# Performance work log

Measured on AMD Instinct MI355X. Metric: run time of the kernel, lower is better.

The kernel has to match this reference:

```python
import jax, jax.numpy as jnp
import numpy as np
from jax import lax

NPOINT = 1024
RADIUS = 0.2
NSAMPLE = 32
BN_EPS = 1e-5


def farthest_point_sample(xyz, npoint):
    # xyz: (B, N, 3). Deterministic start at index 0 (torch uses randint).
    B, N, _ = xyz.shape

    def step(carry, _):
        distance, farthest = carry
        centroid = jnp.take_along_axis(xyz, farthest[:, None, None], axis=1)  # (B,1,3)
        d = jnp.sum((xyz - centroid) ** 2, axis=-1)  # (B,N)
        distance = jnp.minimum(distance, d)
        return (distance, jnp.argmax(distance, axis=-1).astype(jnp.int32)), farthest

    init = (jnp.full((B, N), 1e10, xyz.dtype), jnp.zeros((B,), jnp.int32))
    _, idxs = lax.scan(step, init, None, length=npoint)  # (npoint, B)
    return jnp.transpose(idxs)  # (B, npoint)


def square_distance(src, dst):
    # src: (B,S,3), dst: (B,N,3) -> (B,S,N) squared distances
    d = -2.0 * jnp.einsum('bsc,bnc->bsn', src, dst)
    d = d + jnp.sum(src ** 2, axis=-1)[:, :, None]
    d = d + jnp.sum(dst ** 2, axis=-1)[:, None, :]
    return d


def query_ball_point(radius, nsample, xyz, new_xyz):
    B, N, _ = xyz.shape
    S = new_xyz.shape[1]
    sqrdists = square_distance(new_xyz, xyz)  # (B,S,N)
    idx = jnp.broadcast_to(jnp.arange(N, dtype=jnp.int32), (B, S, N))
    idx = jnp.where(sqrdists > radius ** 2, N, idx)
    idx = jnp.sort(idx, axis=-1)[:, :, :nsample]  # (B,S,K)
    first = idx[:, :, :1]
    return jnp.where(idx == N, first, idx)


# batched gather: points (B,N,C), idx (B,...) -> (B,...,C)
_gather = jax.vmap(lambda p, i: p[i])


def bn_relu(x, gamma, beta):
    # training-mode BatchNorm2d over (B, C, S, K): stats over axes (0,2,3)
    m = jnp.mean(x, axis=(0, 2, 3), keepdims=True)
    v = jnp.var(x, axis=(0, 2, 3), keepdims=True)
    y = (x - m) * lax.rsqrt(v + BN_EPS)
    return jax.nn.relu(y * gamma[None, :, None, None] + beta[None, :, None, None])


def reference(xyz, points, W0, b0, g0, be0, W1, b1, g1, be1, W2, b2, g2, be2):
    # xyz: (B,3,N), points: (B,C,N)
    xyz_t = jnp.transpose(xyz, (0, 2, 1))      # (B,N,3)
    pts_t = jnp.transpose(points, (0, 2, 1))   # (B,N,C)

    fps_idx = farthest_point_sample(xyz_t, NPOINT)          # (B,S)
    new_xyz = _gather(xyz_t, fps_idx)                        # (B,S,3)
    group_idx = query_ball_point(RADIUS, NSAMPLE, xyz_t, new_xyz)  # (B,S,K)

    grouped_xyz = _gather(xyz_t, group_idx) - new_xyz[:, :, None, :]  # (B,S,K,3)
    grouped_pts = _gather(pts_t, group_idx)                           # (B,S,K,C)
    feat = jnp.concatenate([grouped_xyz, grouped_pts], axis=-1)      # (B,S,K,C+3)

    x = jnp.transpose(feat, (0, 3, 1, 2))  # (B, C+3, S, K)
    for W, b, g, be in ((W0, b0, g0, be0), (W1, b1, g1, be1), (W2, b2, g2, be2)):
        x = bn_relu(jnp.einsum('bcsk,oc->bosk', x, W) + b[None, :, None, None], g, be)
    new_points = jnp.max(x, axis=-1)  # (B, C_out, S)

    return jnp.transpose(new_xyz, (0, 2, 1)), new_points


def setup_inputs() -> dict:
    key = jax.random.key(0)
    ks = jax.random.split(key, 8)
    B, C_in, N = 16, 6, 4096
    inp = {
        'xyz': jax.random.uniform(ks[0], (B, 3, N), dtype=jnp.float32),
        'points': jax.random.normal(ks[1], (B, C_in, N), dtype=jnp.float32),
        'W0': 0.1 * jax.random.normal(ks[2], (32, C_in + 3), dtype=jnp.float32),
        'b0': 0.1 * jax.random.normal(ks[3], (32,), dtype=jnp.float32),
        'g0': jnp.ones((32,), jnp.float32),
        'be0': jnp.zeros((32,), jnp.float32),
        'W1': 0.1 * jax.random.normal(ks[4], (32, 32), dtype=jnp.float32),
        'b1': 0.1 * jax.random.normal(ks[5], (32,), dtype=jnp.float32),
        'g1': jnp.ones((32,), jnp.float32),
        'be1': jnp.zeros((32,), jnp.float32),
        'W2': 0.1 * jax.random.normal(ks[6], (64, 32), dtype=jnp.float32),
        'b2': 0.1 * jax.random.normal(ks[7], (64,), dtype=jnp.float32),
        'g2': jnp.ones((64,), jnp.float32),
        'be2': jnp.zeros((64,), jnp.float32),
    }
    return inp
```

## Files before the change

kernel.cpp:

```cpp
#include <hip/hip_runtime.h>

#define BATCH   16
#define NPTS    4096
#define NPOINT  1024
#define NSAMPLE 32
#define NSITES  (BATCH*NPOINT*NSAMPLE)


__device__ __forceinline__ float wave_max_bcast(float x) {
    int v = __float_as_int(x);
    int t;
    t = __builtin_amdgcn_update_dpp(v, v, 0x111, 0xf, 0xf, false);
    v = __float_as_int(fmaxf(__int_as_float(v), __int_as_float(t)));
    t = __builtin_amdgcn_update_dpp(v, v, 0x112, 0xf, 0xf, false);
    v = __float_as_int(fmaxf(__int_as_float(v), __int_as_float(t)));
    t = __builtin_amdgcn_update_dpp(v, v, 0x114, 0xf, 0xf, false);
    v = __float_as_int(fmaxf(__int_as_float(v), __int_as_float(t)));
    t = __builtin_amdgcn_update_dpp(v, v, 0x118, 0xf, 0xf, false);
    v = __float_as_int(fmaxf(__int_as_float(v), __int_as_float(t)));
    t = __builtin_amdgcn_update_dpp(v, v, 0x142, 0xa, 0xf, false);
    v = __float_as_int(fmaxf(__int_as_float(v), __int_as_float(t)));
    t = __builtin_amdgcn_update_dpp(v, v, 0x143, 0xc, 0xf, false);
    v = __float_as_int(fmaxf(__int_as_float(v), __int_as_float(t)));
    return __int_as_float(__builtin_amdgcn_readlane(v, 63));
}

__global__ __launch_bounds__(512, 1) void fps_kernel(
    const float* __restrict__ xyz,
    float* __restrict__ nxyz,
    float* __restrict__ out0)
{
    __shared__ float sx[NPTS], sy[NPTS], sz[NPTS];
    __shared__ int   s_sel[NPOINT];
    __shared__ unsigned long long redK[2][8];

    const int b = blockIdx.x;
    const int t = threadIdx.x;
    const int wave = t >> 6, lane = t & 63;
    const float* xb = xyz + (size_t)b * 3 * NPTS;

    for (int i = t; i < NPTS; i += 512) {
        sx[i] = xb[i]; sy[i] = xb[NPTS+i]; sz[i] = xb[2*NPTS+i];
    }
    __syncthreads();

    const int base = t * 8;
    float px[8], py[8], pz[8], dist[8];
    #pragma unroll
    for (int j = 0; j < 8; ++j) {
        px[j] = sx[base+j]; py[j] = sy[base+j]; pz[j] = sz[base+j];
        dist[j] = 1e10f;
    }

    int far = 0;
    float cx = sx[0], cy = sy[0], cz = sz[0];
    for (int it = 0; it < NPOINT; ++it) {
        if (t == 0) s_sel[it] = far;
        #pragma unroll
        for (int j = 0; j < 8; ++j) {
            const float dx = __fsub_rn(px[j], cx);
            const float dy = __fsub_rn(py[j], cy);
            const float dz = __fsub_rn(pz[j], cz);
            const float d  = __fadd_rn(__fadd_rn(__fmul_rn(dx,dx), __fmul_rn(dy,dy)),
                                       __fmul_rn(dz,dz));
            dist[j] = fminf(dist[j], d);
        }
        float tv0, tv1, tv2, tv3; int ti0, ti1, ti2, ti3;
        { bool c = dist[1] > dist[0]; tv0 = c ? dist[1] : dist[0]; ti0 = c ? 1 : 0; }
        { bool c = dist[3] > dist[2]; tv1 = c ? dist[3] : dist[2]; ti1 = c ? 3 : 2; }
        { bool c = dist[5] > dist[4]; tv2 = c ? dist[5] : dist[4]; ti2 = c ? 5 : 4; }
        { bool c = dist[7] > dist[6]; tv3 = c ? dist[7] : dist[6]; ti3 = c ? 7 : 6; }
        float nv0, nv1; int ni0, ni1;
        { bool c = tv1 > tv0; nv0 = c ? tv1 : tv0; ni0 = c ? ti1 : ti0; }
        { bool c = tv3 > tv2; nv1 = c ? tv3 : tv2; ni1 = c ? ti3 : ti2; }
        float bm; int bj;
        { bool c = nv1 > nv0; bm = c ? nv1 : nv0; bj = c ? ni1 : ni0; }
        const float M = wave_max_bcast(bm);
        const unsigned long long mask = __ballot(bm == M);
        const int wl = __ffsll(mask) - 1;
        const int par = it & 1;
        if (lane == wl) {
            const unsigned idxg = (unsigned)(base + bj);
            redK[par][wave] = ((unsigned long long)__float_as_uint(M) << 32)
                              | (unsigned)(~idxg);
        }
        __syncthreads();
        const unsigned long long k0 = redK[par][0], k1 = redK[par][1];
        const unsigned long long k2 = redK[par][2], k3 = redK[par][3];
        const unsigned long long k4 = redK[par][4], k5 = redK[par][5];
        const unsigned long long k6 = redK[par][6], k7 = redK[par][7];
        const unsigned long long a0 = (k1 > k0) ? k1 : k0;
        const unsigned long long a1 = (k3 > k2) ? k3 : k2;
        const unsigned long long a2 = (k5 > k4) ? k5 : k4;
        const unsigned long long a3 = (k7 > k6) ? k7 : k6;
        const unsigned long long b0_ = (a1 > a0) ? a1 : a0;
        const unsigned long long b1_ = (a3 > a2) ? a3 : a2;
        const unsigned long long km  = (b1_ > b0_) ? b1_ : b0_;
        far = (int)((~(unsigned)km) & (NPTS-1));
        cx = sx[far]; cy = sy[far]; cz = sz[far];
    }
    __syncthreads();
    for (int s = t; s < NPOINT; s += 512) {
        const int id = s_sel[s];
        const float x = sx[id], y = sy[id], z = sz[id];
        nxyz[((size_t)b*NPOINT + s)*3 + 0] = x;
        nxyz[((size_t)b*NPOINT + s)*3 + 1] = y;
        nxyz[((size_t)b*NPOINT + s)*3 + 2] = z;
        out0[(size_t)b*3*NPOINT + 0*NPOINT + s] = x;
        out0[(size_t)b*3*NPOINT + 1*NPOINT + s] = y;
        out0[(size_t)b*3*NPOINT + 2*NPOINT + s] = z;
    }
}

__global__ __launch_bounds__(256) void ball_kernel(
    const float* __restrict__ xyz, const float* __restrict__ nxyz,
    int* __restrict__ gidx)
{
    __shared__ float sx[NPTS], sy[NPTS], sz[NPTS];
    const int b  = blockIdx.x >> 4;
    const int sg = blockIdx.x & 15;
    const int t = threadIdx.x;
    const int wave = t >> 6, lane = t & 63;
    const float* xb = xyz + (size_t)b * 3 * NPTS;
    for (int i = t; i < NPTS; i += 256) {
        sx[i] = xb[i]; sy[i] = xb[NPTS+i]; sz[i] = xb[2*NPTS+i];
    }
    __syncthreads();
    const unsigned long long lt = (1ull << lane) - 1ull;

    for (int q = wave; q < 64; q += 4) {
        const int s = sg*64 + q;
        const size_t bs = (size_t)b*NPOINT + s;
        const float cx = nxyz[bs*3+0], cy = nxyz[bs*3+1], cz = nxyz[bs*3+2];
        const float ss = __fadd_rn(__fadd_rn(__fmul_rn(cx,cx), __fmul_rn(cy,cy)),
                                   __fmul_rn(cz,cz));
        int* out = gidx + bs*NSAMPLE;
        int cnt = 0;
        int firstIdx = NPTS;
        for (int ch = 0; ch < NPTS/64 && cnt < NSAMPLE; ++ch) {
            const int pi = ch*64 + lane;
            const float qx = sx[pi], qy = sy[pi], qz = sz[pi];
            const float dot = fmaf(cz, qz, fmaf(cy, qy, __fmul_rn(cx, qx)));
            const float sn  = __fadd_rn(__fadd_rn(__fmul_rn(qx,qx), __fmul_rn(qy,qy)),
                                        __fmul_rn(qz,qz));
            const float d   = __fadd_rn(__fadd_rn(__fmul_rn(-2.0f,dot), ss), sn);
            const bool pred = !(d > 0.04f);
            const unsigned long long m = __ballot(pred);
            if (pred) {
                const int pos = cnt + __popcll(m & lt);
                if (pos == 0) firstIdx = pi;
                if (pos < NSAMPLE) out[pos] = pi;
            }
            cnt += (int)__popcll(m);
        }
        if (cnt < NSAMPLE) {
            #pragma unroll
            for (int off = 32; off >= 1; off >>= 1) {
                const int oi = __shfl_xor(firstIdx, off);
                firstIdx = (oi < firstIdx) ? oi : firstIdx;
            }
            for (int p = cnt + lane; p < NSAMPLE; p += 64) out[p] = firstIdx;
        }
    }
}

__device__ __forceinline__ void gather_feat(
    const float* __restrict__ xyz, const float* __restrict__ pts,
    const int* __restrict__ gidx, const float* __restrict__ nxyz,
    int v, float4 f[9])
{
    const int site = v * 4;
    const int bs = site >> 5;
    const int b  = bs >> 10;
    const int4 idx = *reinterpret_cast<const int4*>(gidx + site);
    const float* xb = xyz + (size_t)b*3*NPTS;
    const float* pb = pts + (size_t)b*6*NPTS;
    const float cx = nxyz[(size_t)bs*3+0];
    const float cy = nxyz[(size_t)bs*3+1];
    const float cz = nxyz[(size_t)bs*3+2];
    f[0] = make_float4(xb[idx.x]-cx, xb[idx.y]-cx, xb[idx.z]-cx, xb[idx.w]-cx);
    f[1] = make_float4(xb[NPTS+idx.x]-cy, xb[NPTS+idx.y]-cy, xb[NPTS+idx.z]-cy, xb[NPTS+idx.w]-cy);
    f[2] = make_float4(xb[2*NPTS+idx.x]-cz, xb[2*NPTS+idx.y]-cz, xb[2*NPTS+idx.z]-cz, xb[2*NPTS+idx.w]-cz);
    #pragma unroll
    for (int c = 0; c < 6; ++c)
        f[3+c] = make_float4(pb[c*NPTS+idx.x], pb[c*NPTS+idx.y], pb[c*NPTS+idx.z], pb[c*NPTS+idx.w]);
}

__global__ __launch_bounds__(256) void conv0s_kernel(
    const float* __restrict__ xyz, const float* __restrict__ pts,
    const int* __restrict__ gidx, const float* __restrict__ nxyz,
    const float* __restrict__ W, const float* __restrict__ bias,
    float* __restrict__ xout, float* __restrict__ psum, float* __restrict__ psq)
{
    const int t = threadIdx.x;
    const int v = blockIdx.x*256 + t;
    const int site = v * 4;
    float4 f[9];
    gather_feat(xyz, pts, gidx, nxyz, v, f);
    float acc[32], accq[32];
    #pragma unroll
    for (int o = 0; o < 32; ++o) {
        const float bb = bias[o];
        float4 y = make_float4(bb,bb,bb,bb);
        #pragma unroll
        for (int c = 0; c < 9; ++c) {
            const float w = W[o*9+c];
            y.x = fmaf(w, f[c].x, y.x); y.y = fmaf(w, f[c].y, y.y);
            y.z = fmaf(w, f[c].z, y.z); y.w = fmaf(w, f[c].w, y.w);
        }
        *reinterpret_cast<float4*>(xout + (size_t)o*NSITES + site) = y;
        acc[o]  = (y.x + y.y) + (y.z + y.w);
        accq[o] = (y.x*y.x + y.y*y.y) + (y.z*y.z + y.w*y.w);
    }
    __shared__ float ls[4][32], lq[4][32];
    const int wave = t>>6, lane = t&63;
    #pragma unroll
    for (int o = 0; o < 32; ++o) {
        float s1 = acc[o], q1 = accq[o];
        #pragma unroll
        for (int off = 32; off >= 1; off >>= 1) {
            s1 += __shfl_xor(s1, off);
            q1 += __shfl_xor(q1, off);
        }
        if (lane == 0) { ls[wave][o] = s1; lq[wave][o] = q1; }
    }
    __syncthreads();
    if (t < 32) {
        psum[blockIdx.x*64 + t] = (ls[0][t]+ls[1][t]) + (ls[2][t]+ls[3][t]);
        psq [blockIdx.x*64 + t] = (lq[0][t]+lq[1][t]) + (lq[2][t]+lq[3][t]);
    }
}

__global__ void fold_kernel(
    const float* __restrict__ g, const float* __restrict__ be,
    const float* __restrict__ psum, const float* __restrict__ psq,
    float* __restrict__ aff, int Cout)
{
    const int t = threadIdx.x;
    if (t < Cout) {
        float s = 0.f, q = 0.f;
        for (int i = 0; i < 512; ++i) { s += psum[i*64 + t]; q += psq[i*64 + t]; }
        const float invn = 1.0f / (float)NSITES;
        const float m = s * invn;
        float v2 = fmaxf(q * invn - m*m, 0.f);
        const float a = g[t] * rsqrtf(v2 + 1e-5f);
        aff[t]      = a;
        aff[64 + t] = fmaf(-m, a, be[t]);
    }
}

__global__ __launch_bounds__(256) void conv1s_kernel(
    const float* x, float* xout,
    const float* __restrict__ aff, const float* __restrict__ W,
    const float* __restrict__ bias,
    float* __restrict__ psum, float* __restrict__ psq)
{
    const int t = threadIdx.x;
    const int v = blockIdx.x*256 + t;
    const int site = v * 4;
    float4 in[32];
    #pragma unroll
    for (int c = 0; c < 32; ++c) {
        float4 r = *reinterpret_cast<const float4*>(x + (size_t)c*NSITES + site);
        const float a = aff[c], cc = aff[64 + c];
        in[c].x = fmaxf(fmaf(a, r.x, cc), 0.f);
        in[c].y = fmaxf(fmaf(a, r.y, cc), 0.f);
        in[c].z = fmaxf(fmaf(a, r.z, cc), 0.f);
        in[c].w = fmaxf(fmaf(a, r.w, cc), 0.f);
    }
    float acc[32], accq[32];
    #pragma unroll
    for (int o = 0; o < 32; ++o) {
        const float bb = bias[o];
        float4 y = make_float4(bb,bb,bb,bb);
        #pragma unroll
        for (int c = 0; c < 32; ++c) {
            const float w = W[o*32+c];
            y.x = fmaf(w, in[c].x, y.x); y.y = fmaf(w, in[c].y, y.y);
            y.z = fmaf(w, in[c].z, y.z); y.w = fmaf(w, in[c].w, y.w);
        }
        *reinterpret_cast<float4*>(xout + (size_t)o*NSITES + site) = y;
        acc[o]  = (y.x + y.y) + (y.z + y.w);
        accq[o] = (y.x*y.x + y.y*y.y) + (y.z*y.z + y.w*y.w);
    }
    __shared__ float ls[4][32], lq[4][32];
    const int wave = t>>6, lane = t&63;
    #pragma unroll
    for (int o = 0; o < 32; ++o) {
        float s1 = acc[o], q1 = accq[o];
        #pragma unroll
        for (int off = 32; off >= 1; off >>= 1) {
            s1 += __shfl_xor(s1, off);
            q1 += __shfl_xor(q1, off);
        }
        if (lane == 0) { ls[wave][o] = s1; lq[wave][o] = q1; }
    }
    __syncthreads();
    if (t < 32) {
        psum[blockIdx.x*64 + t] = (ls[0][t]+ls[1][t]) + (ls[2][t]+ls[3][t]);
        psq [blockIdx.x*64 + t] = (lq[0][t]+lq[1][t]) + (lq[2][t]+lq[3][t]);
    }
}

__global__ __launch_bounds__(256) void conv2stats_kernel(
    const float* __restrict__ x, const float* __restrict__ aff,
    const float* __restrict__ W, const float* __restrict__ bias,
    float* __restrict__ psum, float* __restrict__ psq)
{
    const int t = threadIdx.x;
    const int v = blockIdx.x*256 + t;
    const int site = v * 4;
    const int coff = blockIdx.y * 32;
    float4 in[32];
    #pragma unroll
    for (int c = 0; c < 32; ++c) {
        float4 r = *reinterpret_cast<const float4*>(x + (size_t)c*NSITES + site);
        const float a = aff[c], cc = aff[64 + c];
        in[c].x = fmaxf(fmaf(a, r.x, cc), 0.f);
        in[c].y = fmaxf(fmaf(a, r.y, cc), 0.f);
        in[c].z = fmaxf(fmaf(a, r.z, cc), 0.f);
        in[c].w = fmaxf(fmaf(a, r.w, cc), 0.f);
    }
    float acc[32], accq[32];
    #pragma unroll
    for (int o = 0; o < 32; ++o) {
        const float bb = bias[coff + o];
        float4 y = make_float4(bb,bb,bb,bb);
        #pragma unroll
        for (int c = 0; c < 32; ++c) {
            const float w = W[(coff+o)*32 + c];
            y.x = fmaf(w, in[c].x, y.x); y.y = fmaf(w, in[c].y, y.y);
            y.z = fmaf(w, in[c].z, y.z); y.w = fmaf(w, in[c].w, y.w);
        }
        acc[o]  = (y.x + y.y) + (y.z + y.w);
        accq[o] = (y.x*y.x + y.y*y.y) + (y.z*y.z + y.w*y.w);
    }
    __shared__ float ls[4][32], lq[4][32];
    const int wave = t>>6, lane = t&63;
    #pragma unroll
    for (int o = 0; o < 32; ++o) {
        float s1 = acc[o], q1 = accq[o];
        #pragma unroll
        for (int off = 32; off >= 1; off >>= 1) {
            s1 += __shfl_xor(s1, off);
            q1 += __shfl_xor(q1, off);
        }
        if (lane == 0) { ls[wave][o] = s1; lq[wave][o] = q1; }
    }
    __syncthreads();
    if (t < 32) {
        psum[blockIdx.x*64 + coff + t] = (ls[0][t]+ls[1][t]) + (ls[2][t]+ls[3][t]);
        psq [blockIdx.x*64 + coff + t] = (lq[0][t]+lq[1][t]) + (lq[2][t]+lq[3][t]);
    }
}

__global__ __launch_bounds__(256) void conv2max_kernel(
    const float* __restrict__ x, const float* __restrict__ aff1,
    const float* __restrict__ aff2, const float* __restrict__ W,
    const float* __restrict__ bias, float* __restrict__ outp)
{
    const int gt = blockIdx.x*256 + threadIdx.x;
    const int wv = gt >> 6;
    const int lane = gt & 63;
    const int base = wv * 64;
    float in[32];
    #pragma unroll
    for (int c = 0; c < 32; ++c) {
        const float r = x[(size_t)c*NSITES + base + lane];
        in[c] = fmaxf(fmaf(aff1[c], r, aff1[64 + c]), 0.f);
    }
    const int bs = (base + lane) >> 5;
    const int b = bs >> 10, s = bs & 1023;
    float* dst = outp + (size_t)b*64*NPOINT + s;
    for (int o = 0; o < 64; ++o) {
        float z = bias[o];
        #pragma unroll
        for (int c = 0; c < 32; ++c)
            z = fmaf(W[o*32+c], in[c], z);
        float y = fmaxf(fmaf(aff2[o], z, aff2[64 + o]), 0.f);
        #pragma unroll
        for (int off = 16; off >= 1; off >>= 1)
            y = fmaxf(y, __shfl_xor(y, off));
        if ((lane & 31) == 0)
            dst[(size_t)o*NPOINT] = y;
    }
}

extern "C" void kernel_launch(void* const* d_in, const int* in_sizes, int n_in,
                              void* d_out, int out_size, void* d_ws, size_t ws_size,
                              hipStream_t stream) {
    (void)in_sizes; (void)n_in; (void)out_size; (void)ws_size;
    const float* xyz = (const float*)d_in[0];
    const float* pts = (const float*)d_in[1];
    const float* W0  = (const float*)d_in[2];
    const float* b0  = (const float*)d_in[3];
    const float* g0  = (const float*)d_in[4];
    const float* be0 = (const float*)d_in[5];
    const float* W1  = (const float*)d_in[6];
    const float* b1  = (const float*)d_in[7];
    const float* g1  = (const float*)d_in[8];
    const float* be1 = (const float*)d_in[9];
    const float* W2  = (const float*)d_in[10];
    const float* b2  = (const float*)d_in[11];
    const float* g2  = (const float*)d_in[12];
    const float* be2 = (const float*)d_in[13];
    float* out = (float*)d_out;
    char* ws = (char*)d_ws;
    float* nxyz = (float*)(ws + 0);
    int*   gidx = (int*)  (ws + 196608);
    float* psum = (float*)(ws + 2293760);
    float* psq  = (float*)(ws + 2424832);
    float* aff0 = (float*)(ws + 2555904);
    float* aff1 = (float*)(ws + 2556416);
    float* aff2 = (float*)(ws + 2556928);
    float* xbuf = (float*)(ws + 2557440);

    fps_kernel <<<16,  512, 0, stream>>>(xyz, nxyz, out);
    ball_kernel<<<256, 256, 0, stream>>>(xyz, nxyz, gidx);

    conv0s_kernel<<<512, 256, 0, stream>>>(xyz, pts, gidx, nxyz, W0, b0,
                                           xbuf, psum, psq);
    fold_kernel<<<1, 64, 0, stream>>>(g0, be0, psum, psq, aff0, 32);

    conv1s_kernel<<<512, 256, 0, stream>>>(xbuf, xbuf, aff0, W1, b1, psum, psq);
    fold_kernel<<<1, 64, 0, stream>>>(g1, be1, psum, psq, aff1, 32);

    conv2stats_kernel<<<dim3(512,2), 256, 0, stream>>>(xbuf, aff1, W2, b2,
                                                       psum, psq);
    fold_kernel<<<1, 64, 0, stream>>>(g2, be2, psum, psq, aff2, 64);

    conv2max_kernel<<<2048, 256, 0, stream>>>(xbuf, aff1, aff2, W2, b2,
                                              out + 49152);
}
```

Baseline: 958.7 us.

## Reduce FPS argmax in one wave and parallelize BN stats fold

```diff
diff --git a/kernel.cpp b/kernel.cpp
--- a/kernel.cpp
+++ b/kernel.cpp
@@ -32,7 +32,8 @@
 {
     __shared__ float sx[NPTS], sy[NPTS], sz[NPTS];
     __shared__ int   s_sel[NPOINT];
-    __shared__ unsigned long long redK[2][8];
+    __shared__ unsigned long long redK[8];
+    __shared__ alignas(16) float bc[4];
 
     const int b = blockIdx.x;
     const int t = threadIdx.x;
@@ -42,6 +43,7 @@
     for (int i = t; i < NPTS; i += 512) {
         sx[i] = xb[i]; sy[i] = xb[NPTS+i]; sz[i] = xb[2*NPTS+i];
     }
+    if (t == 0) s_sel[0] = 0;
     __syncthreads();
 
     const int base = t * 8;
@@ -52,10 +54,8 @@
         dist[j] = 1e10f;
     }
 
-    int far = 0;
     float cx = sx[0], cy = sy[0], cz = sz[0];
     for (int it = 0; it < NPOINT; ++it) {
-        if (t == 0) s_sel[it] = far;
         #pragma unroll
         for (int j = 0; j < 8; ++j) {
             const float dx = __fsub_rn(px[j], cx);
@@ -77,27 +77,35 @@
         { bool c = nv1 > nv0; bm = c ? nv1 : nv0; bj = c ? ni1 : ni0; }
         const float M = wave_max_bcast(bm);
         const unsigned long long mask = __ballot(bm == M);
-        const int wl = __ffsll(mask) - 1;
-        const int par = it & 1;
+        const int wl = __ffsll((long long)mask) - 1;
         if (lane == wl) {
             const unsigned idxg = (unsigned)(base + bj);
-            redK[par][wave] = ((unsigned long long)__float_as_uint(M) << 32)
-                              | (unsigned)(~idxg);
+            redK[wave] = ((unsigned long long)__float_as_uint(bm) << 32)
+                         | (unsigned)(~idxg);
         }
         __syncthreads();
-        const unsigned long long k0 = redK[par][0], k1 = redK[par][1];
-        const unsigned long long k2 = redK[par][2], k3 = redK[par][3];
-        const unsigned long long k4 = redK[par][4], k5 = redK[par][5];
-        const unsigned long long k6 = redK[par][6], k7 = redK[par][7];
-        const unsigned long long a0 = (k1 > k0) ? k1 : k0;
-        const unsigned long long a1 = (k3 > k2) ? k3 : k2;
-        const unsigned long long a2 = (k5 > k4) ? k5 : k4;
-        const unsigned long long a3 = (k7 > k6) ? k7 : k6;
-        const unsigned long long b0_ = (a1 > a0) ? a1 : a0;
-        const unsigned long long b1_ = (a3 > a2) ? a3 : a2;
-        const unsigned long long km  = (b1_ > b0_) ? b1_ : b0_;
-        far = (int)((~(unsigned)km) & (NPTS-1));
-        cx = sx[far]; cy = sy[far]; cz = sz[far];
+        if (wave == 0) {
+            const unsigned long long k0 = redK[0], k1 = redK[1];
+            const unsigned long long k2 = redK[2], k3 = redK[3];
+            const unsigned long long k4 = redK[4], k5 = redK[5];
+            const unsigned long long k6 = redK[6], k7 = redK[7];
+            const unsigned long long a0 = (k1 > k0) ? k1 : k0;
+            const unsigned long long a1 = (k3 > k2) ? k3 : k2;
+            const unsigned long long a2 = (k5 > k4) ? k5 : k4;
+            const unsigned long long a3 = (k7 > k6) ? k7 : k6;
+            const unsigned long long b0_ = (a1 > a0) ? a1 : a0;
+            const unsigned long long b1_ = (a3 > a2) ? a3 : a2;
+            const unsigned long long km  = (b1_ > b0_) ? b1_ : b0_;
+            const int far = (int)((~(unsigned)km) & (NPTS-1));
+            const float fx = sx[far], fy = sy[far], fz = sz[far];
+            if (lane == 0) {
+                if (it + 1 < NPOINT) s_sel[it + 1] = far;
+                *(float4*)bc = make_float4(fx, fy, fz, 0.f);
+            }
+        }
+        __syncthreads();
+        const float4 B = *(const float4*)bc;
+        cx = B.x; cy = B.y; cz = B.z;
     }
     __syncthreads();
     for (int s = t; s < NPOINT; s += 512) {
@@ -236,10 +244,19 @@
     const float* __restrict__ psum, const float* __restrict__ psq,
     float* __restrict__ aff, int Cout)
 {
-    const int t = threadIdx.x;
+    __shared__ float ss[4][64], qq[4][64];
+    const int t = threadIdx.x;
+    const int ch = t & 63, part = t >> 6;
+    float s = 0.f, q = 0.f;
+    for (int i = part; i < 512; i += 4) {
+        s += psum[i*64 + ch];
+        q += psq [i*64 + ch];
+    }
+    ss[part][ch] = s; qq[part][ch] = q;
+    __syncthreads();
     if (t < Cout) {
-        float s = 0.f, q = 0.f;
-        for (int i = 0; i < 512; ++i) { s += psum[i*64 + t]; q += psq[i*64 + t]; }
+        s = (ss[0][t]+ss[1][t]) + (ss[2][t]+ss[3][t]);
+        q = (qq[0][t]+qq[1][t]) + (qq[2][t]+qq[3][t]);
         const float invn = 1.0f / (float)NSITES;
         const float m = s * invn;
         float v2 = fmaxf(q * invn - m*m, 0.f);
@@ -420,14 +437,14 @@
 
     conv0s_kernel<<<512, 256, 0, stream>>>(xyz, pts, gidx, nxyz, W0, b0,
                                            xbuf, psum, psq);
-    fold_kernel<<<1, 64, 0, stream>>>(g0, be0, psum, psq, aff0, 32);
+    fold_kernel<<<1, 256, 0, stream>>>(g0, be0, psum, psq, aff0, 32);
 
     conv1s_kernel<<<512, 256, 0, stream>>>(xbuf, xbuf, aff0, W1, b1, psum, psq);
-    fold_kernel<<<1, 64, 0, stream>>>(g1, be1, psum, psq, aff1, 32);
+    fold_kernel<<<1, 256, 0, stream>>>(g1, be1, psum, psq, aff1, 32);
 
     conv2stats_kernel<<<dim3(512,2), 256, 0, stream>>>(xbuf, aff1, W2, b2,
                                                        psum, psq);
-    fold_kernel<<<1, 64, 0, stream>>>(g2, be2, psum, psq, aff2, 64);
+    fold_kernel<<<1, 256, 0, stream>>>(g2, be2, psum, psq, aff2, 64);
 
     conv2max_kernel<<<2048, 256, 0, stream>>>(xbuf, aff1, aff2, W2, b2,
                                               out + 49152);
```

After: 1.081 ms. +12.8%, slower.
